# Kernel tuning notes

Measured on AMD Instinct MI355X. Metric: run time of the kernel, lower is better.

## Reference

```python
import jax, jax.numpy as jnp
import numpy as np

N = 100000      # nodes
E = 1600000     # directed edges (before self-loops)
F_IN, H1, H2 = 128, 64, 32


def setup_inputs() -> dict:
    key = jax.random.key(0)
    ks = jax.random.split(key, 8)
    x = jax.random.normal(ks[0], (N, F_IN), dtype=jnp.float32)
    edge_index = jax.random.randint(ks[1], (2, E), 0, N, dtype=jnp.int32)
    # GCNConv lin weights (no bias in lin; separate additive bias), glorot-ish scale
    W1 = jax.random.normal(ks[2], (F_IN, H1), dtype=jnp.float32) / np.sqrt(F_IN)
    b1 = jnp.zeros((H1,), dtype=jnp.float32)
    W2 = jax.random.normal(ks[3], (H1, H2), dtype=jnp.float32) / np.sqrt(H1)
    b2 = jnp.zeros((H2,), dtype=jnp.float32)
    Wfc = jax.random.normal(ks[4], (H2, 1), dtype=jnp.float32) / np.sqrt(H2)
    bfc = jnp.zeros((1,), dtype=jnp.float32)
    return {"x": x, "edge_index": edge_index, "W1": W1, "b1": b1,
            "W2": W2, "b2": b2, "Wfc": Wfc, "bfc": bfc}


def _gcn_norm(edge_index):
    # PyG GCNConv default: add self-loops, symmetric normalization D^-1/2 (A+I) D^-1/2
    loop = jnp.arange(N, dtype=edge_index.dtype)
    src = jnp.concatenate([edge_index[0], loop])
    dst = jnp.concatenate([edge_index[1], loop])
    deg = jax.ops.segment_sum(jnp.ones_like(dst, dtype=jnp.float32), dst, num_segments=N)
    dinv = jnp.where(deg > 0, jax.lax.rsqrt(deg), 0.0)
    norm = dinv[src] * dinv[dst]  # [E+N]
    return src, dst, norm


def _gcn_conv(x, W, b, src, dst, norm):
    h = x @ W                                 # project first (PyG order)
    msg = norm[:, None] * h[src]              # gather + scale
    agg = jax.ops.segment_sum(msg, dst, num_segments=N)  # scatter-add
    return agg + b


def reference(x, edge_index, W1, b1, W2, b2, Wfc, bfc):
    src, dst, norm = _gcn_norm(edge_index)
    h = jax.nn.relu(_gcn_conv(x, W1, b1, src, dst, norm))
    h = jax.nn.relu(_gcn_conv(h, W2, b2, src, dst, norm))
    return h @ Wfc + bfc
```

## Files before the change

### kernel.cpp

```cpp
#include <hip/hip_runtime.h>

#define N_NODES 100000
#define BSH 9
#define NBKT ((N_NODES + 511) >> BSH)
#define CH 7168

typedef unsigned int u32;
typedef unsigned short u16;
typedef __attribute__((ext_vector_type(8))) short s8v;
typedef __attribute__((ext_vector_type(4))) float f4v;

static __device__ __forceinline__ u16 f2bf(float f) {
    union { float f; u32 u; } c; c.f = f;
    u32 r = (c.u + 0x7fffu + ((c.u >> 16) & 1u)) >> 16;
    return (u16)r;
}
static __device__ __forceinline__ float bf2f_u(u16 h) {
    union { u32 u; float f; } c; c.u = ((u32)h) << 16;
    return c.f;
}
static __device__ __forceinline__ void acc2(u32 p, float& a, float& b) {
    union { u32 u; float f; } lo, hi;
    lo.u = p << 16;
    hi.u = p & 0xffff0000u;
    a += lo.f;
    b += hi.f;
}


__global__ __launch_bounds__(256) void coarsehist_k(const int* __restrict__ dst,
        int* __restrict__ ccount, int E, int TOT) {
    __shared__ int hist[256];
    hist[threadIdx.x] = 0;
    __syncthreads();
    int base = blockIdx.x * CH;
    int cnt = min(CH, TOT - base);
    for (int i = threadIdx.x; i < cnt; i += 256) {
        int e = base + i;
        int d = (e < E) ? dst[e] : e - E;
        atomicAdd(&hist[d >> BSH], 1);
    }
    __syncthreads();
    if (hist[threadIdx.x]) atomicAdd(&ccount[threadIdx.x], hist[threadIdx.x]);
}

__global__ __launch_bounds__(256) void coarsescan_k(const int* __restrict__ ccount,
        int* __restrict__ cbase, int* __restrict__ bcur, int* __restrict__ offsets) {
    __shared__ int ps[256];
    int t = threadIdx.x;
    int c = (t < NBKT) ? ccount[t] : 0;
    ps[t] = c;
    __syncthreads();
    for (int off = 1; off < 256; off <<= 1) {
        int val = ps[t];
        int add = (t >= off) ? ps[t - off] : 0;
        __syncthreads();
        ps[t] = val + add;
        __syncthreads();
    }
    int incl = ps[t], excl = incl - c;
    if (t < NBKT) cbase[t] = excl;
    bcur[t] = (t < NBKT) ? excl : incl;
    if (t == NBKT - 1) cbase[NBKT] = incl;
    if (t == 255) offsets[N_NODES] = ps[255];
}

__global__ __launch_bounds__(256) void partition_k(const int* __restrict__ src,
        const int* __restrict__ dst, int* __restrict__ bcur,
        uint2* __restrict__ bktBuf, int E, int TOT) {
    __shared__ int hist[256];
    __shared__ int lbase[256];
    __shared__ int gbase[256];
    __shared__ int ps[256];
    __shared__ uint2 stage[CH];
    int t = threadIdx.x;
    int base = blockIdx.x * CH;
    int cnt = min(CH, TOT - base);
    hist[t] = 0;
    __syncthreads();
    for (int i = t; i < cnt; i += 256) {
        int e = base + i;
        int d = (e < E) ? dst[e] : e - E;
        atomicAdd(&hist[d >> BSH], 1);
    }
    __syncthreads();
    ps[t] = hist[t];
    __syncthreads();
    for (int off = 1; off < 256; off <<= 1) {
        int val = ps[t];
        int add = (t >= off) ? ps[t - off] : 0;
        __syncthreads();
        ps[t] = val + add;
        __syncthreads();
    }
    lbase[t] = ps[t] - hist[t];
    gbase[t] = atomicAdd(&bcur[t], hist[t]);
    hist[t] = 0;
    __syncthreads();
    for (int i = t; i < cnt; i += 256) {
        int e = base + i;
        int s, d;
        if (e < E) { s = src[e]; d = dst[e]; }
        else       { s = d = e - E; }
        int b = d >> BSH;
        int lpos = lbase[b] + atomicAdd(&hist[b], 1);
        stage[lpos] = make_uint2((u32)s, (u32)d);
    }
    __syncthreads();
    for (int i = t; i < cnt; i += 256) {
        uint2 p = stage[i];
        int b = (int)p.y >> BSH;
        bktBuf[gbase[b] + (i - lbase[b])] = p;
    }
}

__global__ __launch_bounds__(256) void buildfill_k(const int* __restrict__ cbase,
        const uint2* __restrict__ bktBuf, int* __restrict__ offsets,
        float* __restrict__ dinv, int* __restrict__ srt_src) {
    __shared__ int hist[512];
    __shared__ int hscan[512];
    __shared__ int cur[512];
    __shared__ int ps[256];
    int t = threadIdx.x;
    int b = blockIdx.x;
    int v0 = b << BSH;
    int nv = min(512, N_NODES - v0);
    hist[t] = 0; hist[t + 256] = 0;
    cur[t] = 0;  cur[t + 256] = 0;
    __syncthreads();
    int beg = cbase[b], endi = cbase[b + 1];
    for (int i = beg + t; i < endi; i += 256)
        atomicAdd(&hist[(int)bktBuf[i].y - v0], 1);
    __syncthreads();
    int a = hist[2 * t], bb = hist[2 * t + 1];
    int own = a + bb;
    ps[t] = own;
    __syncthreads();
    for (int off = 1; off < 256; off <<= 1) {
        int val = ps[t];
        int add = (t >= off) ? ps[t - off] : 0;
        __syncthreads();
        ps[t] = val + add;
        __syncthreads();
    }
    int excl2 = ps[t] - own;
    hscan[2 * t] = excl2;
    hscan[2 * t + 1] = excl2 + a;
    __syncthreads();
    for (int j = t; j < nv; j += 256) {
        offsets[v0 + j] = beg + hscan[j];
        dinv[v0 + j] = rsqrtf((float)hist[j]);
    }
    for (int i = beg + t; i < endi; i += 256) {
        uint2 p = bktBuf[i];
        int j = (int)p.y - v0;
        int pos = atomicAdd(&cur[j], 1);
        srt_src[beg + hscan[j] + pos] = (int)p.x;
    }
}


static __device__ __forceinline__ void split8(const float* __restrict__ xp,
                                              s8v& hi, s8v& lo) {
    float4 v0 = *(const float4*)xp;
    float4 v1 = *(const float4*)(xp + 4);
    float xv[8] = {v0.x, v0.y, v0.z, v0.w, v1.x, v1.y, v1.z, v1.w};
#pragma unroll
    for (int j = 0; j < 8; ++j) {
        u16 h = f2bf(xv[j]);
        hi[j] = (short)h;
        lo[j] = (short)f2bf(xv[j] - bf2f_u(h));
    }
}

__global__ __launch_bounds__(256) void gemm1_k(const float* __restrict__ x,
                                               const float* __restrict__ W1,
                                               const float* __restrict__ dinv,
                                               u16* __restrict__ h1b) {
    __shared__ __attribute__((aligned(16))) short Bs[2][4][4][512];
    int t = threadIdx.x;
    for (int i = t; i < 128 * 64; i += 256) {
        int k = i >> 6, c = i & 63;
        float w = W1[i];
        u16 h = f2bf(w);
        u16 l = f2bf(w - bf2f_u(h));
        int ks = k >> 5, kg = (k >> 3) & 3, kk = k & 7;
        int ct = c >> 4, col = c & 15;
        int idx = (kg * 16 + col) * 8 + kk;
        Bs[0][ks][ct][idx] = (short)h;
        Bs[1][ks][ct][idx] = (short)l;
    }
    __syncthreads();

    int lane = t & 63;
    int rows0 = (blockIdx.x * 4 + (t >> 6)) * 32;
    if (rows0 >= N_NODES) return;

    f4v acc[2][4];
#pragma unroll
    for (int rt = 0; rt < 2; ++rt)
#pragma unroll
        for (int ct = 0; ct < 4; ++ct)
            acc[rt][ct] = (f4v){0.f, 0.f, 0.f, 0.f};

    int arow = lane & 15;
    int kgl = lane >> 4;
#pragma unroll
    for (int ks = 0; ks < 4; ++ks) {
        s8v bh[4], bl[4];
#pragma unroll
        for (int ct = 0; ct < 4; ++ct) {
            bh[ct] = *(const s8v*)&Bs[0][ks][ct][lane * 8];
            bl[ct] = *(const s8v*)&Bs[1][ks][ct][lane * 8];
        }
#pragma unroll
        for (int rt = 0; rt < 2; ++rt) {
            s8v ah, al;
            const float* xp = x + (size_t)(rows0 + rt * 16 + arow) * 128
                                + ks * 32 + kgl * 8;
            split8(xp, ah, al);
#pragma unroll
            for (int ct = 0; ct < 4; ++ct) {
                acc[rt][ct] = __builtin_amdgcn_mfma_f32_16x16x32_bf16(
                    ah, bh[ct], acc[rt][ct], 0, 0, 0);
                acc[rt][ct] = __builtin_amdgcn_mfma_f32_16x16x32_bf16(
                    ah, bl[ct], acc[rt][ct], 0, 0, 0);
                acc[rt][ct] = __builtin_amdgcn_mfma_f32_16x16x32_bf16(
                    al, bh[ct], acc[rt][ct], 0, 0, 0);
            }
        }
    }

#pragma unroll
    for (int rt = 0; rt < 2; ++rt) {
        int rbase = rows0 + rt * 16 + ((lane >> 4) << 2);
        float dv[4];
#pragma unroll
        for (int r = 0; r < 4; ++r) dv[r] = dinv[rbase + r];
#pragma unroll
        for (int ct = 0; ct < 4; ++ct) {
            int col = ct * 16 + (lane & 15);
#pragma unroll
            for (int r = 0; r < 4; ++r)
                h1b[(size_t)(rbase + r) * 64 + col] = f2bf(acc[rt][ct][r] * dv[r]);
        }
    }
}


__global__ __launch_bounds__(256) void layer2_k(const int* __restrict__ offsets,
        const int* __restrict__ srt_src, const float* __restrict__ dinv,
        const u16* __restrict__ h1b, const float* __restrict__ b1,
        const float* __restrict__ W2, u16* __restrict__ h2b) {
    __shared__ float W2s[64 * 32];
    __shared__ float b1s[64];
    for (int i = threadIdx.x; i < 64 * 32; i += 256) W2s[i] = W2[i];
    if (threadIdx.x < 64) b1s[threadIdx.x] = b1[threadIdx.x];
    __syncthreads();
    int lane = threadIdx.x & 63;
    int f = lane & 15, q = lane >> 4;
    int v0 = blockIdx.x * 8 + (threadIdx.x >> 6) * 2;
    int v1 = v0 + 1;
    int i0 = offsets[v0], e0 = offsets[v1], e1 = offsets[v1 + 1];
    int i1 = e0;
    const uint2* rows = (const uint2*)h1b;
    float a0 = 0.f, a1 = 0.f, a2 = 0.f, a3 = 0.f;
    float c0 = 0.f, c1 = 0.f, c2 = 0.f, c3 = 0.f;
    while (i0 + 8 <= e0 && i1 + 8 <= e1) {
        int sA = srt_src[i0 + q];
        int sB = srt_src[i0 + 4 + q];
        int sC = srt_src[i1 + q];
        int sD = srt_src[i1 + 4 + q];
        uint2 pA = rows[sA * 16 + f];
        uint2 pB = rows[sB * 16 + f];
        uint2 pC = rows[sC * 16 + f];
        uint2 pD = rows[sD * 16 + f];
        acc2(pA.x, a0, a1); acc2(pA.y, a2, a3);
        acc2(pB.x, a0, a1); acc2(pB.y, a2, a3);
        acc2(pC.x, c0, c1); acc2(pC.y, c2, c3);
        acc2(pD.x, c0, c1); acc2(pD.y, c2, c3);
        i0 += 8; i1 += 8;
    }
    for (; i0 + 8 <= e0; i0 += 8) {
        int sA = srt_src[i0 + q], sB = srt_src[i0 + 4 + q];
        uint2 pA = rows[sA * 16 + f], pB = rows[sB * 16 + f];
        acc2(pA.x, a0, a1); acc2(pA.y, a2, a3);
        acc2(pB.x, a0, a1); acc2(pB.y, a2, a3);
    }
    for (; i0 < e0; i0 += 4) {
        int j = i0 + q;
        if (j < e0) {
            int s = srt_src[j];
            uint2 p = rows[s * 16 + f];
            acc2(p.x, a0, a1); acc2(p.y, a2, a3);
        }
    }
    for (; i1 + 8 <= e1; i1 += 8) {
        int sA = srt_src[i1 + q], sB = srt_src[i1 + 4 + q];
        uint2 pA = rows[sA * 16 + f], pB = rows[sB * 16 + f];
        acc2(pA.x, c0, c1); acc2(pA.y, c2, c3);
        acc2(pB.x, c0, c1); acc2(pB.y, c2, c3);
    }
    for (; i1 < e1; i1 += 4) {
        int j = i1 + q;
        if (j < e1) {
            int s = srt_src[j];
            uint2 p = rows[s * 16 + f];
            acc2(p.x, c0, c1); acc2(p.y, c2, c3);
        }
    }
    a0 += __shfl_xor(a0, 16, 64); a0 += __shfl_xor(a0, 32, 64);
    a1 += __shfl_xor(a1, 16, 64); a1 += __shfl_xor(a1, 32, 64);
    a2 += __shfl_xor(a2, 16, 64); a2 += __shfl_xor(a2, 32, 64);
    a3 += __shfl_xor(a3, 16, 64); a3 += __shfl_xor(a3, 32, 64);
    c0 += __shfl_xor(c0, 16, 64); c0 += __shfl_xor(c0, 32, 64);
    c1 += __shfl_xor(c1, 16, 64); c1 += __shfl_xor(c1, 32, 64);
    c2 += __shfl_xor(c2, 16, 64); c2 += __shfl_xor(c2, 32, 64);
    c3 += __shfl_xor(c3, 16, 64); c3 += __shfl_xor(c3, 32, 64);
    bool lo = (lane < 32);
    float dv = lo ? dinv[v0] : dinv[v1];
    float t0 = lo ? a0 : c0;
    float t1 = lo ? a1 : c1;
    float t2 = lo ? a2 : c2;
    float t3 = lo ? a3 : c3;
    float r0 = fmaxf(fmaf(dv, t0, b1s[4 * f + 0]), 0.f);
    float r1 = fmaxf(fmaf(dv, t1, b1s[4 * f + 1]), 0.f);
    float r2 = fmaxf(fmaf(dv, t2, b1s[4 * f + 2]), 0.f);
    float r3 = fmaxf(fmaf(dv, t3, b1s[4 * f + 3]), 0.f);
    int c = lane & 31;
    float o = 0.f;
#pragma unroll
    for (int j2 = 0; j2 < 16; ++j2) {
        float R0 = __shfl(r0, j2, 16);
        float R1 = __shfl(r1, j2, 16);
        float R2 = __shfl(r2, j2, 16);
        float R3 = __shfl(r3, j2, 16);
        o = fmaf(R0, W2s[(4 * j2 + 0) * 32 + c], o);
        o = fmaf(R1, W2s[(4 * j2 + 1) * 32 + c], o);
        o = fmaf(R2, W2s[(4 * j2 + 2) * 32 + c], o);
        o = fmaf(R3, W2s[(4 * j2 + 3) * 32 + c], o);
    }
    int vst = lo ? v0 : v1;
    h2b[vst * 32 + c] = f2bf(dv * o);
}


#define GATH3(ii, A, B, C, D) { \
    int s_ = srt_src[(ii) + oc]; \
    uint2 p_ = rows[s_ * 8 + f]; \
    acc2(p_.x, A, B); acc2(p_.y, C, D); }

__global__ __launch_bounds__(256) void layer3_k(const int* __restrict__ offsets,
        const int* __restrict__ srt_src, const float* __restrict__ dinv,
        const u16* __restrict__ h2b, const float* __restrict__ b2,
        const float* __restrict__ Wfc, const float* __restrict__ bfc,
        float* __restrict__ out) {
    int lane = threadIdx.x & 63;
    int f = lane & 7, oc = lane >> 3;
    int vb = blockIdx.x * 16 + (threadIdx.x >> 6) * 4;
    int o0 = offsets[vb], o1 = offsets[vb + 1], o2 = offsets[vb + 2];
    int o3 = offsets[vb + 3], o4 = offsets[vb + 4];
    int i0 = o0, e0 = o1, i1 = o1, e1 = o2, i2 = o2, e2 = o3, i3 = o3, e3 = o4;
    const uint2* rows = (const uint2*)h2b;
    float A0=0.f,A1=0.f,A2=0.f,A3=0.f, B0=0.f,B1=0.f,B2=0.f,B3=0.f;
    float C0=0.f,C1=0.f,C2=0.f,C3=0.f, D0=0.f,D1=0.f,D2=0.f,D3=0.f;
    while (i0 + 8 <= e0 && i1 + 8 <= e1 && i2 + 8 <= e2 && i3 + 8 <= e3) {
        GATH3(i0, A0, A1, A2, A3);
        GATH3(i1, B0, B1, B2, B3);
        GATH3(i2, C0, C1, C2, C3);
        GATH3(i3, D0, D1, D2, D3);
        i0 += 8; i1 += 8; i2 += 8; i3 += 8;
    }
    while (i0 + 8 <= e0) { GATH3(i0, A0, A1, A2, A3); i0 += 8; }
    if (i0 + oc < e0)    { GATH3(i0, A0, A1, A2, A3); }
    while (i1 + 8 <= e1) { GATH3(i1, B0, B1, B2, B3); i1 += 8; }
    if (i1 + oc < e1)    { GATH3(i1, B0, B1, B2, B3); }
    while (i2 + 8 <= e2) { GATH3(i2, C0, C1, C2, C3); i2 += 8; }
    if (i2 + oc < e2)    { GATH3(i2, C0, C1, C2, C3); }
    while (i3 + 8 <= e3) { GATH3(i3, D0, D1, D2, D3); i3 += 8; }
    if (i3 + oc < e3)    { GATH3(i3, D0, D1, D2, D3); }
#define RED3(X) X += __shfl_xor(X, 8, 64); X += __shfl_xor(X, 16, 64); X += __shfl_xor(X, 32, 64)
    RED3(A0); RED3(A1); RED3(A2); RED3(A3);
    RED3(B0); RED3(B1); RED3(B2); RED3(B3);
    RED3(C0); RED3(C1); RED3(C2); RED3(C3);
    RED3(D0); RED3(D1); RED3(D2); RED3(D3);
    float w0 = Wfc[4 * f + 0], w1 = Wfc[4 * f + 1];
    float w2 = Wfc[4 * f + 2], w3 = Wfc[4 * f + 3];
    float g0 = b2[4 * f + 0], g1 = b2[4 * f + 1];
    float g2 = b2[4 * f + 2], g3 = b2[4 * f + 3];
    float dv0 = dinv[vb], dv1 = dinv[vb + 1], dv2 = dinv[vb + 2], dv3 = dinv[vb + 3];
    float p0 = fmaxf(fmaf(dv0, A0, g0), 0.f) * w0 + fmaxf(fmaf(dv0, A1, g1), 0.f) * w1
             + fmaxf(fmaf(dv0, A2, g2), 0.f) * w2 + fmaxf(fmaf(dv0, A3, g3), 0.f) * w3;
    float p1 = fmaxf(fmaf(dv1, B0, g0), 0.f) * w0 + fmaxf(fmaf(dv1, B1, g1), 0.f) * w1
             + fmaxf(fmaf(dv1, B2, g2), 0.f) * w2 + fmaxf(fmaf(dv1, B3, g3), 0.f) * w3;
    float p2 = fmaxf(fmaf(dv2, C0, g0), 0.f) * w0 + fmaxf(fmaf(dv2, C1, g1), 0.f) * w1
             + fmaxf(fmaf(dv2, C2, g2), 0.f) * w2 + fmaxf(fmaf(dv2, C3, g3), 0.f) * w3;
    float p3 = fmaxf(fmaf(dv3, D0, g0), 0.f) * w0 + fmaxf(fmaf(dv3, D1, g1), 0.f) * w1
             + fmaxf(fmaf(dv3, D2, g2), 0.f) * w2 + fmaxf(fmaf(dv3, D3, g3), 0.f) * w3;
#define REDP(X) X += __shfl_xor(X, 1, 64); X += __shfl_xor(X, 2, 64); X += __shfl_xor(X, 4, 64)
    REDP(p0); REDP(p1); REDP(p2); REDP(p3);
    if (lane == 0) {
        float bb = bfc[0];
        out[vb + 0] = p0 + bb;
        out[vb + 1] = p1 + bb;
        out[vb + 2] = p2 + bb;
        out[vb + 3] = p3 + bb;
    }
}


extern "C" void kernel_launch(void* const* d_in, const int* in_sizes, int n_in,
                              void* d_out, int out_size, void* d_ws, size_t ws_size,
                              hipStream_t stream) {
    const float* x   = (const float*)d_in[0];
    const int*   ei  = (const int*)d_in[1];
    const float* W1  = (const float*)d_in[2];
    const float* b1  = (const float*)d_in[3];
    const float* W2  = (const float*)d_in[4];
    const float* b2  = (const float*)d_in[5];
    const float* Wfc = (const float*)d_in[6];
    const float* bfc = (const float*)d_in[7];
    float* out = (float*)d_out;

    const int E = in_sizes[1] / 2;
    const int TOT = E + N_NODES;
    const int* src = ei;
    const int* dst = ei + E;

    int*   ccount  = (int*)d_ws;
    int*   cbase   = ccount + 256;
    int*   bcur    = cbase + 256;
    int*   offsets = bcur + 256;
    int*   srt_src = offsets + N_NODES + 1;
    size_t bb_off  = (size_t)(srt_src - (int*)d_ws) + TOT;
    bb_off = (bb_off + 1) & ~(size_t)1;
    uint2* bktBuf  = (uint2*)((int*)d_ws + bb_off);
    float* dinv    = (float*)((int*)d_ws + bb_off + 2 * (size_t)TOT);
    u16*   h1b     = (u16*)(dinv + N_NODES);
    u16*   h2b     = h1b + (size_t)N_NODES * 64;

    const int NCH = (TOT + CH - 1) / CH;

    hipMemsetAsync(ccount, 0, 256 * sizeof(int), stream);
    coarsehist_k<<<NCH, 256, 0, stream>>>(dst, ccount, E, TOT);
    coarsescan_k<<<1, 256, 0, stream>>>(ccount, cbase, bcur, offsets);
    partition_k<<<NCH, 256, 0, stream>>>(src, dst, bcur, bktBuf, E, TOT);
    buildfill_k<<<NBKT, 256, 0, stream>>>(cbase, bktBuf, offsets, dinv, srt_src);

    const int GB1 = (N_NODES / 32 + 3) / 4;
    gemm1_k<<<GB1, 256, 0, stream>>>(x, W1, dinv, h1b);

    layer2_k<<<N_NODES / 8, 256, 0, stream>>>(offsets, srt_src, dinv, h1b, b1, W2, h2b);
    layer3_k<<<N_NODES / 16, 256, 0, stream>>>(offsets, srt_src, dinv, h2b, b2, Wfc,
                                               bfc, out);
}
```

Before: 210.2 us.

## Widen gathers to 16-byte loads and software-pipeline edge fetches in aggregation kernels

Layer2 and layer3 gather kernels now load bf16 feature rows as uint4 (8 bf16 per lane) instead of uint2, so each wave covers more edges per iteration (8 in layer2, 16 in layer3). A register double-buffer prefetches the next gather before accumulating the current one, keeping more loads in flight. The intent is to cut instruction count and hide gather latency. It costs more registers and larger shuffle reductions, which may lower occupancy and waste lanes on low-degree nodes.

```diff
diff --git a/kernel.cpp b/kernel.cpp
--- a/kernel.cpp
+++ b/kernel.cpp
@@ -25,6 +25,10 @@
     hi.u = p & 0xffff0000u;
     a += lo.f;
     b += hi.f;
+}
+static __device__ __forceinline__ void acc8(uint4 p, float* a) {
+    acc2(p.x, a[0], a[1]); acc2(p.y, a[2], a[3]);
+    acc2(p.z, a[4], a[5]); acc2(p.w, a[6], a[7]);
 }
 
 
@@ -248,6 +252,10 @@
 }
 
 
+#define L2_FETCH(F, V, P, EE) \
+    if (P + 8 <= EE) { int s_ = srt_src[P + oc8]; F = rows4[s_ * 8 + f8]; \
+                       V = true; P += 8; } else V = false;
+
 __global__ __launch_bounds__(256) void layer2_k(const int* __restrict__ offsets,
         const int* __restrict__ srt_src, const float* __restrict__ dinv,
         const u16* __restrict__ h1b, const float* __restrict__ b1,
@@ -258,97 +266,71 @@
     if (threadIdx.x < 64) b1s[threadIdx.x] = b1[threadIdx.x];
     __syncthreads();
     int lane = threadIdx.x & 63;
-    int f = lane & 15, q = lane >> 4;
+    int f8 = lane & 7, oc8 = lane >> 3;
     int v0 = blockIdx.x * 8 + (threadIdx.x >> 6) * 2;
     int v1 = v0 + 1;
-    int i0 = offsets[v0], e0 = offsets[v1], e1 = offsets[v1 + 1];
-    int i1 = e0;
-    const uint2* rows = (const uint2*)h1b;
-    float a0 = 0.f, a1 = 0.f, a2 = 0.f, a3 = 0.f;
-    float c0 = 0.f, c1 = 0.f, c2 = 0.f, c3 = 0.f;
-    while (i0 + 8 <= e0 && i1 + 8 <= e1) {
-        int sA = srt_src[i0 + q];
-        int sB = srt_src[i0 + 4 + q];
-        int sC = srt_src[i1 + q];
-        int sD = srt_src[i1 + 4 + q];
-        uint2 pA = rows[sA * 16 + f];
-        uint2 pB = rows[sB * 16 + f];
-        uint2 pC = rows[sC * 16 + f];
-        uint2 pD = rows[sD * 16 + f];
-        acc2(pA.x, a0, a1); acc2(pA.y, a2, a3);
-        acc2(pB.x, a0, a1); acc2(pB.y, a2, a3);
-        acc2(pC.x, c0, c1); acc2(pC.y, c2, c3);
-        acc2(pD.x, c0, c1); acc2(pD.y, c2, c3);
-        i0 += 8; i1 += 8;
-    }
-    for (; i0 + 8 <= e0; i0 += 8) {
-        int sA = srt_src[i0 + q], sB = srt_src[i0 + 4 + q];
-        uint2 pA = rows[sA * 16 + f], pB = rows[sB * 16 + f];
-        acc2(pA.x, a0, a1); acc2(pA.y, a2, a3);
-        acc2(pB.x, a0, a1); acc2(pB.y, a2, a3);
-    }
-    for (; i0 < e0; i0 += 4) {
-        int j = i0 + q;
-        if (j < e0) {
-            int s = srt_src[j];
-            uint2 p = rows[s * 16 + f];
-            acc2(p.x, a0, a1); acc2(p.y, a2, a3);
-        }
-    }
-    for (; i1 + 8 <= e1; i1 += 8) {
-        int sA = srt_src[i1 + q], sB = srt_src[i1 + 4 + q];
-        uint2 pA = rows[sA * 16 + f], pB = rows[sB * 16 + f];
-        acc2(pA.x, c0, c1); acc2(pA.y, c2, c3);
-        acc2(pB.x, c0, c1); acc2(pB.y, c2, c3);
-    }
-    for (; i1 < e1; i1 += 4) {
-        int j = i1 + q;
-        if (j < e1) {
-            int s = srt_src[j];
-            uint2 p = rows[s * 16 + f];
-            acc2(p.x, c0, c1); acc2(p.y, c2, c3);
-        }
-    }
-    a0 += __shfl_xor(a0, 16, 64); a0 += __shfl_xor(a0, 32, 64);
-    a1 += __shfl_xor(a1, 16, 64); a1 += __shfl_xor(a1, 32, 64);
-    a2 += __shfl_xor(a2, 16, 64); a2 += __shfl_xor(a2, 32, 64);
-    a3 += __shfl_xor(a3, 16, 64); a3 += __shfl_xor(a3, 32, 64);
-    c0 += __shfl_xor(c0, 16, 64); c0 += __shfl_xor(c0, 32, 64);
-    c1 += __shfl_xor(c1, 16, 64); c1 += __shfl_xor(c1, 32, 64);
-    c2 += __shfl_xor(c2, 16, 64); c2 += __shfl_xor(c2, 32, 64);
-    c3 += __shfl_xor(c3, 16, 64); c3 += __shfl_xor(c3, 32, 64);
+    int p0 = offsets[v0], e0 = offsets[v1], e1 = offsets[v1 + 1];
+    int p1 = e0;
+    const uint4* rows4 = (const uint4*)h1b;
+    float a[8] = {0.f, 0.f, 0.f, 0.f, 0.f, 0.f, 0.f, 0.f};
+    float c[8] = {0.f, 0.f, 0.f, 0.f, 0.f, 0.f, 0.f, 0.f};
+    uint4 F0a, F0b, F1a, F1b;
+    bool v0a, v0b, v1a, v1b;
+    L2_FETCH(F0a, v0a, p0, e0);
+    L2_FETCH(F1a, v1a, p1, e1);
+    L2_FETCH(F0b, v0b, p0, e0);
+    L2_FETCH(F1b, v1b, p1, e1);
+    while (v0a || v1a) {
+        uint4 C0 = F0a, C1 = F1a;
+        bool c0 = v0a, c1 = v1a;
+        F0a = F0b; v0a = v0b;
+        F1a = F1b; v1a = v1b;
+        L2_FETCH(F0b, v0b, p0, e0);
+        L2_FETCH(F1b, v1b, p1, e1);
+        if (c0) acc8(C0, a);
+        if (c1) acc8(C1, c);
+    }
+    if (p0 + oc8 < e0) {
+        int s_ = srt_src[p0 + oc8];
+        acc8(rows4[s_ * 8 + f8], a);
+    }
+    if (p1 + oc8 < e1) {
+        int s_ = srt_src[p1 + oc8];
+        acc8(rows4[s_ * 8 + f8], c);
+    }
+#pragma unroll
+    for (int j = 0; j < 8; ++j) {
+        a[j] += __shfl_xor(a[j], 8, 64);
+        a[j] += __shfl_xor(a[j], 16, 64);
+        a[j] += __shfl_xor(a[j], 32, 64);
+        c[j] += __shfl_xor(c[j], 8, 64);
+        c[j] += __shfl_xor(c[j], 16, 64);
+        c[j] += __shfl_xor(c[j], 32, 64);
+    }
     bool lo = (lane < 32);
     float dv = lo ? dinv[v0] : dinv[v1];
-    float t0 = lo ? a0 : c0;
-    float t1 = lo ? a1 : c1;
-    float t2 = lo ? a2 : c2;
-    float t3 = lo ? a3 : c3;
-    float r0 = fmaxf(fmaf(dv, t0, b1s[4 * f + 0]), 0.f);
-    float r1 = fmaxf(fmaf(dv, t1, b1s[4 * f + 1]), 0.f);
-    float r2 = fmaxf(fmaf(dv, t2, b1s[4 * f + 2]), 0.f);
-    float r3 = fmaxf(fmaf(dv, t3, b1s[4 * f + 3]), 0.f);
-    int c = lane & 31;
+    float r[8];
+#pragma unroll
+    for (int j = 0; j < 8; ++j) {
+        float tv = lo ? a[j] : c[j];
+        r[j] = fmaxf(fmaf(dv, tv, b1s[8 * f8 + j]), 0.f);
+    }
+    int cc = lane & 31;
     float o = 0.f;
 #pragma unroll
-    for (int j2 = 0; j2 < 16; ++j2) {
-        float R0 = __shfl(r0, j2, 16);
-        float R1 = __shfl(r1, j2, 16);
-        float R2 = __shfl(r2, j2, 16);
-        float R3 = __shfl(r3, j2, 16);
-        o = fmaf(R0, W2s[(4 * j2 + 0) * 32 + c], o);
-        o = fmaf(R1, W2s[(4 * j2 + 1) * 32 + c], o);
-        o = fmaf(R2, W2s[(4 * j2 + 2) * 32 + c], o);
-        o = fmaf(R3, W2s[(4 * j2 + 3) * 32 + c], o);
+    for (int g = 0; g < 8; ++g) {
+#pragma unroll
+        for (int j = 0; j < 8; ++j)
+            o = fmaf(__shfl(r[j], g, 8), W2s[(8 * g + j) * 32 + cc], o);
     }
     int vst = lo ? v0 : v1;
-    h2b[vst * 32 + c] = f2bf(dv * o);
-}
-
-
-#define GATH3(ii, A, B, C, D) { \
-    int s_ = srt_src[(ii) + oc]; \
-    uint2 p_ = rows[s_ * 8 + f]; \
-    acc2(p_.x, A, B); acc2(p_.y, C, D); }
+    h2b[vst * 32 + cc] = f2bf(dv * o);
+}
+
+
+#define L3_FETCH(F, V, P, EE) \
+    if (P + 16 <= EE) { int s_ = srt_src[P + sl]; F = rows4[s_ * 4 + f4]; \
+                        V = true; P += 16; } else V = false;
 
 __global__ __launch_bounds__(256) void layer3_k(const int* __restrict__ offsets,
         const int* __restrict__ srt_src, const float* __restrict__ dinv,
@@ -356,55 +338,70 @@
         const float* __restrict__ Wfc, const float* __restrict__ bfc,
         float* __restrict__ out) {
     int lane = threadIdx.x & 63;
-    int f = lane & 7, oc = lane >> 3;
+    int f4 = lane & 3, sl = lane >> 2;
     int vb = blockIdx.x * 16 + (threadIdx.x >> 6) * 4;
     int o0 = offsets[vb], o1 = offsets[vb + 1], o2 = offsets[vb + 2];
     int o3 = offsets[vb + 3], o4 = offsets[vb + 4];
-    int i0 = o0, e0 = o1, i1 = o1, e1 = o2, i2 = o2, e2 = o3, i3 = o3, e3 = o4;
-    const uint2* rows = (const uint2*)h2b;
-    float A0=0.f,A1=0.f,A2=0.f,A3=0.f, B0=0.f,B1=0.f,B2=0.f,B3=0.f;
-    float C0=0.f,C1=0.f,C2=0.f,C3=0.f, D0=0.f,D1=0.f,D2=0.f,D3=0.f;
-    while (i0 + 8 <= e0 && i1 + 8 <= e1 && i2 + 8 <= e2 && i3 + 8 <= e3) {
-        GATH3(i0, A0, A1, A2, A3);
-        GATH3(i1, B0, B1, B2, B3);
-        GATH3(i2, C0, C1, C2, C3);
-        GATH3(i3, D0, D1, D2, D3);
-        i0 += 8; i1 += 8; i2 += 8; i3 += 8;
-    }
-    while (i0 + 8 <= e0) { GATH3(i0, A0, A1, A2, A3); i0 += 8; }
-    if (i0 + oc < e0)    { GATH3(i0, A0, A1, A2, A3); }
-    while (i1 + 8 <= e1) { GATH3(i1, B0, B1, B2, B3); i1 += 8; }
-    if (i1 + oc < e1)    { GATH3(i1, B0, B1, B2, B3); }
-    while (i2 + 8 <= e2) { GATH3(i2, C0, C1, C2, C3); i2 += 8; }
-    if (i2 + oc < e2)    { GATH3(i2, C0, C1, C2, C3); }
-    while (i3 + 8 <= e3) { GATH3(i3, D0, D1, D2, D3); i3 += 8; }
-    if (i3 + oc < e3)    { GATH3(i3, D0, D1, D2, D3); }
-#define RED3(X) X += __shfl_xor(X, 8, 64); X += __shfl_xor(X, 16, 64); X += __shfl_xor(X, 32, 64)
-    RED3(A0); RED3(A1); RED3(A2); RED3(A3);
-    RED3(B0); RED3(B1); RED3(B2); RED3(B3);
-    RED3(C0); RED3(C1); RED3(C2); RED3(C3);
-    RED3(D0); RED3(D1); RED3(D2); RED3(D3);
-    float w0 = Wfc[4 * f + 0], w1 = Wfc[4 * f + 1];
-    float w2 = Wfc[4 * f + 2], w3 = Wfc[4 * f + 3];
-    float g0 = b2[4 * f + 0], g1 = b2[4 * f + 1];
-    float g2 = b2[4 * f + 2], g3 = b2[4 * f + 3];
+    int p0 = o0, e0 = o1, p1 = o1, e1 = o2, p2 = o2, e2 = o3, p3 = o3, e3 = o4;
+    const uint4* rows4 = (const uint4*)h2b;
+    float A[8] = {0.f, 0.f, 0.f, 0.f, 0.f, 0.f, 0.f, 0.f};
+    float B[8] = {0.f, 0.f, 0.f, 0.f, 0.f, 0.f, 0.f, 0.f};
+    float C[8] = {0.f, 0.f, 0.f, 0.f, 0.f, 0.f, 0.f, 0.f};
+    float D[8] = {0.f, 0.f, 0.f, 0.f, 0.f, 0.f, 0.f, 0.f};
+    uint4 F0, F1, F2, F3;
+    bool g0, g1, g2, g3;
+    L3_FETCH(F0, g0, p0, e0);
+    L3_FETCH(F1, g1, p1, e1);
+    L3_FETCH(F2, g2, p2, e2);
+    L3_FETCH(F3, g3, p3, e3);
+    while (g0 || g1 || g2 || g3) {
+        uint4 T0 = F0, T1 = F1, T2 = F2, T3 = F3;
+        bool h0 = g0, h1 = g1, h2 = g2, h3 = g3;
+        L3_FETCH(F0, g0, p0, e0);
+        L3_FETCH(F1, g1, p1, e1);
+        L3_FETCH(F2, g2, p2, e2);
+        L3_FETCH(F3, g3, p3, e3);
+        if (h0) acc8(T0, A);
+        if (h1) acc8(T1, B);
+        if (h2) acc8(T2, C);
+        if (h3) acc8(T3, D);
+    }
+    if (p0 + sl < e0) { int s_ = srt_src[p0 + sl]; acc8(rows4[s_ * 4 + f4], A); }
+    if (p1 + sl < e1) { int s_ = srt_src[p1 + sl]; acc8(rows4[s_ * 4 + f4], B); }
+    if (p2 + sl < e2) { int s_ = srt_src[p2 + sl]; acc8(rows4[s_ * 4 + f4], C); }
+    if (p3 + sl < e3) { int s_ = srt_src[p3 + sl]; acc8(rows4[s_ * 4 + f4], D); }
+#pragma unroll
+    for (int j = 0; j < 8; ++j) {
+        A[j] += __shfl_xor(A[j], 4, 64);  A[j] += __shfl_xor(A[j], 8, 64);
+        A[j] += __shfl_xor(A[j], 16, 64); A[j] += __shfl_xor(A[j], 32, 64);
+        B[j] += __shfl_xor(B[j], 4, 64);  B[j] += __shfl_xor(B[j], 8, 64);
+        B[j] += __shfl_xor(B[j], 16, 64); B[j] += __shfl_xor(B[j], 32, 64);
+        C[j] += __shfl_xor(C[j], 4, 64);  C[j] += __shfl_xor(C[j], 8, 64);
+        C[j] += __shfl_xor(C[j], 16, 64); C[j] += __shfl_xor(C[j], 32, 64);
+        D[j] += __shfl_xor(D[j], 4, 64);  D[j] += __shfl_xor(D[j], 8, 64);
+        D[j] += __shfl_xor(D[j], 16, 64); D[j] += __shfl_xor(D[j], 32, 64);
+    }
     float dv0 = dinv[vb], dv1 = dinv[vb + 1], dv2 = dinv[vb + 2], dv3 = dinv[vb + 3];
-    float p0 = fmaxf(fmaf(dv0, A0, g0), 0.f) * w0 + fmaxf(fmaf(dv0, A1, g1), 0.f) * w1
-             + fmaxf(fmaf(dv0, A2, g2), 0.f) * w2 + fmaxf(fmaf(dv0, A3, g3), 0.f) * w3;
-    float p1 = fmaxf(fmaf(dv1, B0, g0), 0.f) * w0 + fmaxf(fmaf(dv1, B1, g1), 0.f) * w1
-             + fmaxf(fmaf(dv1, B2, g2), 0.f) * w2 + fmaxf(fmaf(dv1, B3, g3), 0.f) * w3;
-    float p2 = fmaxf(fmaf(dv2, C0, g0), 0.f) * w0 + fmaxf(fmaf(dv2, C1, g1), 0.f) * w1
-             + fmaxf(fmaf(dv2, C2, g2), 0.f) * w2 + fmaxf(fmaf(dv2, C3, g3), 0.f) * w3;
-    float p3 = fmaxf(fmaf(dv3, D0, g0), 0.f) * w0 + fmaxf(fmaf(dv3, D1, g1), 0.f) * w1
-             + fmaxf(fmaf(dv3, D2, g2), 0.f) * w2 + fmaxf(fmaf(dv3, D3, g3), 0.f) * w3;
-#define REDP(X) X += __shfl_xor(X, 1, 64); X += __shfl_xor(X, 2, 64); X += __shfl_xor(X, 4, 64)
-    REDP(p0); REDP(p1); REDP(p2); REDP(p3);
+    float pr0 = 0.f, pr1 = 0.f, pr2 = 0.f, pr3 = 0.f;
+#pragma unroll
+    for (int j = 0; j < 8; ++j) {
+        int k = 8 * f4 + j;
+        float w = Wfc[k], g = b2[k];
+        pr0 += fmaxf(fmaf(dv0, A[j], g), 0.f) * w;
+        pr1 += fmaxf(fmaf(dv1, B[j], g), 0.f) * w;
+        pr2 += fmaxf(fmaf(dv2, C[j], g), 0.f) * w;
+        pr3 += fmaxf(fmaf(dv3, D[j], g), 0.f) * w;
+    }
+    pr0 += __shfl_xor(pr0, 1, 64); pr0 += __shfl_xor(pr0, 2, 64);
+    pr1 += __shfl_xor(pr1, 1, 64); pr1 += __shfl_xor(pr1, 2, 64);
+    pr2 += __shfl_xor(pr2, 1, 64); pr2 += __shfl_xor(pr2, 2, 64);
+    pr3 += __shfl_xor(pr3, 1, 64); pr3 += __shfl_xor(pr3, 2, 64);
     if (lane == 0) {
         float bb = bfc[0];
-        out[vb + 0] = p0 + bb;
-        out[vb + 1] = p1 + bb;
-        out[vb + 2] = p2 + bb;
-        out[vb + 3] = p3 + bb;
+        out[vb + 0] = pr0 + bb;
+        out[vb + 1] = pr1 + bb;
+        out[vb + 2] = pr2 + bb;
+        out[vb + 3] = pr3 + bb;
     }
 }
 
```

Measured after the change: 226.3 us. 1.08x slower.

## Split layer-2 aggregation into source-range segments for cache locality

Applied to the files above, without the earlier changes.

Sorts each node's incoming edges by source segment (src>>15, four segments) during CSR build. The layer-2 gather then runs one pass per segment, with blocks interleaved so concurrently running blocks read from the same quarter of h1b and hit in L2 more often. Each pass writes bf16 partial sums, and a new finalize kernel adds the four partials, applies bias, ReLU and the W2 projection. The cost is an extra partial buffer of roughly 51MB, an extra kernel launch, larger shared histograms in buildfill, and an extra bf16 rounding of the partial sums.

```diff
diff --git a/kernel.cpp b/kernel.cpp
--- a/kernel.cpp
+++ b/kernel.cpp
@@ -4,6 +4,8 @@
 #define BSH 9
 #define NBKT ((N_NODES + 511) >> BSH)
 #define CH 7168
+#define SEGSH 15
+#define NSEG 4
 
 typedef unsigned int u32;
 typedef unsigned short u16;
@@ -25,6 +27,10 @@
     hi.u = p & 0xffff0000u;
     a += lo.f;
     b += hi.f;
+}
+static __device__ __forceinline__ void acc8(uint4 p, float* a) {
+    acc2(p.x, a[0], a[1]); acc2(p.y, a[2], a[3]);
+    acc2(p.z, a[4], a[5]); acc2(p.w, a[6], a[7]);
 }
 
 
@@ -116,24 +122,28 @@
 
 __global__ __launch_bounds__(256) void buildfill_k(const int* __restrict__ cbase,
         const uint2* __restrict__ bktBuf, int* __restrict__ offsets,
-        float* __restrict__ dinv, int* __restrict__ srt_src) {
-    __shared__ int hist[512];
-    __shared__ int hscan[512];
-    __shared__ int cur[512];
+        int* __restrict__ soff, float* __restrict__ dinv,
+        int* __restrict__ srt_src) {
+    __shared__ int hist[2048];
+    __shared__ int hscan[2048];
+    __shared__ int cur[2048];
     __shared__ int ps[256];
     int t = threadIdx.x;
     int b = blockIdx.x;
     int v0 = b << BSH;
     int nv = min(512, N_NODES - v0);
-    hist[t] = 0; hist[t + 256] = 0;
-    cur[t] = 0;  cur[t + 256] = 0;
+    for (int k = t; k < 2048; k += 256) { hist[k] = 0; cur[k] = 0; }
     __syncthreads();
     int beg = cbase[b], endi = cbase[b + 1];
-    for (int i = beg + t; i < endi; i += 256)
-        atomicAdd(&hist[(int)bktBuf[i].y - v0], 1);
-    __syncthreads();
-    int a = hist[2 * t], bb = hist[2 * t + 1];
-    int own = a + bb;
+    for (int i = beg + t; i < endi; i += 256) {
+        uint2 p = bktBuf[i];
+        atomicAdd(&hist[(((int)p.y - v0) << 2) | ((int)p.x >> SEGSH)], 1);
+    }
+    __syncthreads();
+    int loc[8];
+    int own = 0;
+#pragma unroll
+    for (int k = 0; k < 8; ++k) { loc[k] = hist[8 * t + k]; own += loc[k]; }
     ps[t] = own;
     __syncthreads();
     for (int off = 1; off < 256; off <<= 1) {
@@ -143,19 +153,24 @@
         ps[t] = val + add;
         __syncthreads();
     }
-    int excl2 = ps[t] - own;
-    hscan[2 * t] = excl2;
-    hscan[2 * t + 1] = excl2 + a;
+    int run = ps[t] - own;
+#pragma unroll
+    for (int k = 0; k < 8; ++k) { hscan[8 * t + k] = run; run += loc[k]; }
     __syncthreads();
     for (int j = t; j < nv; j += 256) {
-        offsets[v0 + j] = beg + hscan[j];
-        dinv[v0 + j] = rsqrtf((float)hist[j]);
+        int h4 = j << 2;
+        offsets[v0 + j] = beg + hscan[h4];
+#pragma unroll
+        for (int s = 0; s < 4; ++s)
+            soff[(size_t)(v0 + j) * 4 + s] = beg + hscan[h4 + s];
+        dinv[v0 + j] = rsqrtf((float)(hist[h4] + hist[h4 + 1]
+                                      + hist[h4 + 2] + hist[h4 + 3]));
     }
     for (int i = beg + t; i < endi; i += 256) {
         uint2 p = bktBuf[i];
-        int j = (int)p.y - v0;
-        int pos = atomicAdd(&cur[j], 1);
-        srt_src[beg + hscan[j] + pos] = (int)p.x;
+        int j2 = (((int)p.y - v0) << 2) | ((int)p.x >> SEGSH);
+        int pos = atomicAdd(&cur[j2], 1);
+        srt_src[beg + hscan[j2] + pos] = (int)p.x;
     }
 }
 
@@ -248,66 +263,52 @@
 }
 
 
-__global__ __launch_bounds__(256) void layer2_k(const int* __restrict__ offsets,
-        const int* __restrict__ srt_src, const float* __restrict__ dinv,
-        const u16* __restrict__ h1b, const float* __restrict__ b1,
-        const float* __restrict__ W2, u16* __restrict__ h2b) {
-    __shared__ float W2s[64 * 32];
-    __shared__ float b1s[64];
-    for (int i = threadIdx.x; i < 64 * 32; i += 256) W2s[i] = W2[i];
-    if (threadIdx.x < 64) b1s[threadIdx.x] = b1[threadIdx.x];
-    __syncthreads();
-    int lane = threadIdx.x & 63;
+__global__ __launch_bounds__(256) void aggseg_k(const int* __restrict__ soff,
+        const int* __restrict__ offsets, const int* __restrict__ srt_src,
+        const u16* __restrict__ h1b, u16* __restrict__ partial) {
+    int t = threadIdx.x, lane = t & 63;
+    int b = blockIdx.x;
+    int r = b & 7;
+    int seg = r >> 1;
+    int ng = (b >> 3) * 2 + (r & 1);
+    int v0 = ng * 8 + (t >> 6) * 2;
+    int v1 = v0 + 1;
     int f = lane & 15, q = lane >> 4;
-    int v0 = blockIdx.x * 8 + (threadIdx.x >> 6) * 2;
-    int v1 = v0 + 1;
-    int i0 = offsets[v0], e0 = offsets[v1], e1 = offsets[v1 + 1];
-    int i1 = e0;
+    int i0 = soff[(size_t)v0 * 4 + seg];
+    int e0 = (seg < 3) ? soff[(size_t)v0 * 4 + seg + 1] : offsets[v0 + 1];
+    int i1 = soff[(size_t)v1 * 4 + seg];
+    int e1 = (seg < 3) ? soff[(size_t)v1 * 4 + seg + 1] : offsets[v1 + 1];
     const uint2* rows = (const uint2*)h1b;
     float a0 = 0.f, a1 = 0.f, a2 = 0.f, a3 = 0.f;
     float c0 = 0.f, c1 = 0.f, c2 = 0.f, c3 = 0.f;
-    while (i0 + 8 <= e0 && i1 + 8 <= e1) {
+    while (i0 + 4 <= e0 && i1 + 4 <= e1) {
         int sA = srt_src[i0 + q];
-        int sB = srt_src[i0 + 4 + q];
         int sC = srt_src[i1 + q];
-        int sD = srt_src[i1 + 4 + q];
         uint2 pA = rows[sA * 16 + f];
-        uint2 pB = rows[sB * 16 + f];
         uint2 pC = rows[sC * 16 + f];
-        uint2 pD = rows[sD * 16 + f];
         acc2(pA.x, a0, a1); acc2(pA.y, a2, a3);
-        acc2(pB.x, a0, a1); acc2(pB.y, a2, a3);
         acc2(pC.x, c0, c1); acc2(pC.y, c2, c3);
-        acc2(pD.x, c0, c1); acc2(pD.y, c2, c3);
-        i0 += 8; i1 += 8;
-    }
-    for (; i0 + 8 <= e0; i0 += 8) {
-        int sA = srt_src[i0 + q], sB = srt_src[i0 + 4 + q];
-        uint2 pA = rows[sA * 16 + f], pB = rows[sB * 16 + f];
-        acc2(pA.x, a0, a1); acc2(pA.y, a2, a3);
-        acc2(pB.x, a0, a1); acc2(pB.y, a2, a3);
-    }
-    for (; i0 < e0; i0 += 4) {
-        int j = i0 + q;
-        if (j < e0) {
-            int s = srt_src[j];
-            uint2 p = rows[s * 16 + f];
-            acc2(p.x, a0, a1); acc2(p.y, a2, a3);
-        }
-    }
-    for (; i1 + 8 <= e1; i1 += 8) {
-        int sA = srt_src[i1 + q], sB = srt_src[i1 + 4 + q];
-        uint2 pA = rows[sA * 16 + f], pB = rows[sB * 16 + f];
-        acc2(pA.x, c0, c1); acc2(pA.y, c2, c3);
-        acc2(pB.x, c0, c1); acc2(pB.y, c2, c3);
-    }
-    for (; i1 < e1; i1 += 4) {
-        int j = i1 + q;
-        if (j < e1) {
-            int s = srt_src[j];
-            uint2 p = rows[s * 16 + f];
-            acc2(p.x, c0, c1); acc2(p.y, c2, c3);
-        }
+        i0 += 4; i1 += 4;
+    }
+    for (; i0 + 4 <= e0; i0 += 4) {
+        int s = srt_src[i0 + q];
+        uint2 p = rows[s * 16 + f];
+        acc2(p.x, a0, a1); acc2(p.y, a2, a3);
+    }
+    if (i0 + q < e0) {
+        int s = srt_src[i0 + q];
+        uint2 p = rows[s * 16 + f];
+        acc2(p.x, a0, a1); acc2(p.y, a2, a3);
+    }
+    for (; i1 + 4 <= e1; i1 += 4) {
+        int s = srt_src[i1 + q];
+        uint2 p = rows[s * 16 + f];
+        acc2(p.x, c0, c1); acc2(p.y, c2, c3);
+    }
+    if (i1 + q < e1) {
+        int s = srt_src[i1 + q];
+        uint2 p = rows[s * 16 + f];
+        acc2(p.x, c0, c1); acc2(p.y, c2, c3);
     }
     a0 += __shfl_xor(a0, 16, 64); a0 += __shfl_xor(a0, 32, 64);
     a1 += __shfl_xor(a1, 16, 64); a1 += __shfl_xor(a1, 32, 64);
@@ -318,30 +319,51 @@
     c2 += __shfl_xor(c2, 16, 64); c2 += __shfl_xor(c2, 32, 64);
     c3 += __shfl_xor(c3, 16, 64); c3 += __shfl_xor(c3, 32, 64);
     bool lo = (lane < 32);
-    float dv = lo ? dinv[v0] : dinv[v1];
+    int v = lo ? v0 : v1;
     float t0 = lo ? a0 : c0;
     float t1 = lo ? a1 : c1;
     float t2 = lo ? a2 : c2;
     float t3 = lo ? a3 : c3;
-    float r0 = fmaxf(fmaf(dv, t0, b1s[4 * f + 0]), 0.f);
-    float r1 = fmaxf(fmaf(dv, t1, b1s[4 * f + 1]), 0.f);
-    float r2 = fmaxf(fmaf(dv, t2, b1s[4 * f + 2]), 0.f);
-    float r3 = fmaxf(fmaf(dv, t3, b1s[4 * f + 3]), 0.f);
-    int c = lane & 31;
+    if ((lane & 31) < 16) {
+        u32 xw = (u32)f2bf(t0) | ((u32)f2bf(t1) << 16);
+        u32 yw = (u32)f2bf(t2) | ((u32)f2bf(t3) << 16);
+        ((uint2*)partial)[((size_t)seg * N_NODES + v) * 16 + (lane & 15)] =
+            make_uint2(xw, yw);
+    }
+}
+
+
+__global__ __launch_bounds__(256) void l2fin_k(const u16* __restrict__ partial,
+        const float* __restrict__ dinv, const float* __restrict__ b1,
+        const float* __restrict__ W2, u16* __restrict__ h2b) {
+    __shared__ float W2s[64 * 32];
+    __shared__ float b1s[64];
+    for (int i = threadIdx.x; i < 64 * 32; i += 256) W2s[i] = W2[i];
+    if (threadIdx.x < 64) b1s[threadIdx.x] = b1[threadIdx.x];
+    __syncthreads();
+    int t = threadIdx.x, lane = t & 63;
+    int half = lane >> 5, fl = lane & 31;
+    int v = blockIdx.x * 8 + (t >> 6) * 2 + half;
+    const u32* prow = (const u32*)partial;
+    float r0 = 0.f, r1 = 0.f;
+#pragma unroll
+    for (int s = 0; s < 4; ++s) {
+        u32 u = prow[((size_t)s * N_NODES + v) * 32 + fl];
+        r0 += bf2f_u((u16)(u & 0xffff));
+        r1 += bf2f_u((u16)(u >> 16));
+    }
+    float dv = dinv[v];
+    r0 = fmaxf(fmaf(dv, r0, b1s[2 * fl]), 0.f);
+    r1 = fmaxf(fmaf(dv, r1, b1s[2 * fl + 1]), 0.f);
     float o = 0.f;
 #pragma unroll
-    for (int j2 = 0; j2 < 16; ++j2) {
-        float R0 = __shfl(r0, j2, 16);
-        float R1 = __shfl(r1, j2, 16);
-        float R2 = __shfl(r2, j2, 16);
-        float R3 = __shfl(r3, j2, 16);
-        o = fmaf(R0, W2s[(4 * j2 + 0) * 32 + c], o);
-        o = fmaf(R1, W2s[(4 * j2 + 1) * 32 + c], o);
-        o = fmaf(R2, W2s[(4 * j2 + 2) * 32 + c], o);
-        o = fmaf(R3, W2s[(4 * j2 + 3) * 32 + c], o);
-    }
-    int vst = lo ? v0 : v1;
-    h2b[vst * 32 + c] = f2bf(dv * o);
+    for (int g = 0; g < 32; ++g) {
+        float R0 = __shfl(r0, g, 32);
+        float R1 = __shfl(r1, g, 32);
+        o = fmaf(R0, W2s[(2 * g) * 32 + fl], o);
+        o = fmaf(R1, W2s[(2 * g + 1) * 32 + fl], o);
+    }
+    h2b[(size_t)v * 32 + fl] = f2bf(dv * o);
 }
 
 
@@ -431,13 +453,14 @@
     int*   cbase   = ccount + 256;
     int*   bcur    = cbase + 256;
     int*   offsets = bcur + 256;
-    int*   srt_src = offsets + N_NODES + 1;
-    size_t bb_off  = (size_t)(srt_src - (int*)d_ws) + TOT;
-    bb_off = (bb_off + 1) & ~(size_t)1;
-    uint2* bktBuf  = (uint2*)((int*)d_ws + bb_off);
-    float* dinv    = (float*)((int*)d_ws + bb_off + 2 * (size_t)TOT);
+    int*   soff    = offsets + N_NODES + 1;
+    int*   srt_src = soff + 4 * N_NODES;
+    float* dinv    = (float*)(srt_src + TOT);
     u16*   h1b     = (u16*)(dinv + N_NODES);
     u16*   h2b     = h1b + (size_t)N_NODES * 64;
+    size_t tail = ((size_t)(h2b + (size_t)N_NODES * 32 - (u16*)d_ws) + 3) & ~(size_t)3;
+    u16*   partial = (u16*)d_ws + tail;
+    uint2* bktBuf  = (uint2*)partial;
 
     const int NCH = (TOT + CH - 1) / CH;
 
@@ -445,12 +468,14 @@
     coarsehist_k<<<NCH, 256, 0, stream>>>(dst, ccount, E, TOT);
     coarsescan_k<<<1, 256, 0, stream>>>(ccount, cbase, bcur, offsets);
     partition_k<<<NCH, 256, 0, stream>>>(src, dst, bcur, bktBuf, E, TOT);
-    buildfill_k<<<NBKT, 256, 0, stream>>>(cbase, bktBuf, offsets, dinv, srt_src);
+    buildfill_k<<<NBKT, 256, 0, stream>>>(cbase, bktBuf, offsets, soff, dinv, srt_src);
 
     const int GB1 = (N_NODES / 32 + 3) / 4;
     gemm1_k<<<GB1, 256, 0, stream>>>(x, W1, dinv, h1b);
 
-    layer2_k<<<N_NODES / 8, 256, 0, stream>>>(offsets, srt_src, dinv, h1b, b1, W2, h2b);
+    aggseg_k<<<NSEG * (N_NODES / 8), 256, 0, stream>>>(soff, offsets, srt_src,
+                                                       h1b, partial);
+    l2fin_k<<<N_NODES / 8, 256, 0, stream>>>(partial, dinv, b1, W2, h2b);
     layer3_k<<<N_NODES / 16, 256, 0, stream>>>(offsets, srt_src, dinv, h2b, b2, Wfc,
                                                bfc, out);
 }
```

Measured after the change: 252.9 us. +20.3%, slower.

## Replace coarse histogram pass with fixed-slack buckets and pack edge pairs

Applied to the files above, without the earlier changes.

Drops the coarse histogram kernel, the scan kernel and the memset. Each destination bucket now gets a fixed SLACK-sized region, so partitioning needs one pass over the edges instead of two. Bucket entries are packed into one 32-bit word (9-bit local dst plus 17-bit src) instead of a uint2, which halves bucket-buffer traffic. Because the CSR now has gaps between buckets, per-node end indices are stored and used by the aggregation kernels. This relies on no bucket overflowing 10240 entries, which holds for uniformly random inputs but is not guaranteed in general.

```diff
diff --git a/kernel.cpp b/kernel.cpp
--- a/kernel.cpp
+++ b/kernel.cpp
@@ -4,9 +4,11 @@
 #define BSH 9
 #define NBKT ((N_NODES + 511) >> BSH)
 #define CH 7168
+#define SLACK 10240
 
 typedef unsigned int u32;
 typedef unsigned short u16;
+typedef unsigned char u8;
 typedef __attribute__((ext_vector_type(8))) short s8v;
 typedef __attribute__((ext_vector_type(4))) float f4v;
 
@@ -26,53 +28,25 @@
     a += lo.f;
     b += hi.f;
 }
-
-
-__global__ __launch_bounds__(256) void coarsehist_k(const int* __restrict__ dst,
-        int* __restrict__ ccount, int E, int TOT) {
-    __shared__ int hist[256];
-    hist[threadIdx.x] = 0;
-    __syncthreads();
-    int base = blockIdx.x * CH;
-    int cnt = min(CH, TOT - base);
-    for (int i = threadIdx.x; i < cnt; i += 256) {
-        int e = base + i;
-        int d = (e < E) ? dst[e] : e - E;
-        atomicAdd(&hist[d >> BSH], 1);
-    }
-    __syncthreads();
-    if (hist[threadIdx.x]) atomicAdd(&ccount[threadIdx.x], hist[threadIdx.x]);
-}
-
-__global__ __launch_bounds__(256) void coarsescan_k(const int* __restrict__ ccount,
-        int* __restrict__ cbase, int* __restrict__ bcur, int* __restrict__ offsets) {
-    __shared__ int ps[256];
-    int t = threadIdx.x;
-    int c = (t < NBKT) ? ccount[t] : 0;
-    ps[t] = c;
-    __syncthreads();
-    for (int off = 1; off < 256; off <<= 1) {
-        int val = ps[t];
-        int add = (t >= off) ? ps[t - off] : 0;
-        __syncthreads();
-        ps[t] = val + add;
-        __syncthreads();
-    }
-    int incl = ps[t], excl = incl - c;
-    if (t < NBKT) cbase[t] = excl;
-    bcur[t] = (t < NBKT) ? excl : incl;
-    if (t == NBKT - 1) cbase[NBKT] = incl;
-    if (t == 255) offsets[N_NODES] = ps[255];
+static __device__ __forceinline__ void acc8(uint4 p, float* a) {
+    acc2(p.x, a[0], a[1]); acc2(p.y, a[2], a[3]);
+    acc2(p.z, a[4], a[5]); acc2(p.w, a[6], a[7]);
+}
+
+
+__global__ __launch_bounds__(256) void initcur_k(int* __restrict__ bcur) {
+    bcur[threadIdx.x] = threadIdx.x * SLACK;
 }
 
 __global__ __launch_bounds__(256) void partition_k(const int* __restrict__ src,
         const int* __restrict__ dst, int* __restrict__ bcur,
-        uint2* __restrict__ bktBuf, int E, int TOT) {
+        u32* __restrict__ bktBuf, int E, int TOT) {
     __shared__ int hist[256];
     __shared__ int lbase[256];
     __shared__ int gbase[256];
     __shared__ int ps[256];
-    __shared__ uint2 stage[CH];
+    __shared__ u32 stage[CH];
+    __shared__ u8 stageB[CH];
     int t = threadIdx.x;
     int base = blockIdx.x * CH;
     int cnt = min(CH, TOT - base);
@@ -104,19 +78,20 @@
         else       { s = d = e - E; }
         int b = d >> BSH;
         int lpos = lbase[b] + atomicAdd(&hist[b], 1);
-        stage[lpos] = make_uint2((u32)s, (u32)d);
+        stage[lpos] = ((u32)(d & 511) << 17) | (u32)s;
+        stageB[lpos] = (u8)b;
     }
     __syncthreads();
     for (int i = t; i < cnt; i += 256) {
-        uint2 p = stage[i];
-        int b = (int)p.y >> BSH;
-        bktBuf[gbase[b] + (i - lbase[b])] = p;
-    }
-}
-
-__global__ __launch_bounds__(256) void buildfill_k(const int* __restrict__ cbase,
-        const uint2* __restrict__ bktBuf, int* __restrict__ offsets,
-        float* __restrict__ dinv, int* __restrict__ srt_src) {
+        int b = stageB[i];
+        bktBuf[gbase[b] + (i - lbase[b])] = stage[i];
+    }
+}
+
+__global__ __launch_bounds__(256) void buildfill_k(const int* __restrict__ bcur,
+        const u32* __restrict__ bktBuf, int* __restrict__ offsets,
+        int* __restrict__ ends, float* __restrict__ dinv,
+        int* __restrict__ srt_src) {
     __shared__ int hist[512];
     __shared__ int hscan[512];
     __shared__ int cur[512];
@@ -125,12 +100,13 @@
     int b = blockIdx.x;
     int v0 = b << BSH;
     int nv = min(512, N_NODES - v0);
+    int base = b * SLACK;
+    int cnt = bcur[b] - base;
     hist[t] = 0; hist[t + 256] = 0;
     cur[t] = 0;  cur[t + 256] = 0;
     __syncthreads();
-    int beg = cbase[b], endi = cbase[b + 1];
-    for (int i = beg + t; i < endi; i += 256)
-        atomicAdd(&hist[(int)bktBuf[i].y - v0], 1);
+    for (int i = t; i < cnt; i += 256)
+        atomicAdd(&hist[bktBuf[base + i] >> 17], 1);
     __syncthreads();
     int a = hist[2 * t], bb = hist[2 * t + 1];
     int own = a + bb;
@@ -148,14 +124,16 @@
     hscan[2 * t + 1] = excl2 + a;
     __syncthreads();
     for (int j = t; j < nv; j += 256) {
-        offsets[v0 + j] = beg + hscan[j];
+        int o = base + hscan[j];
+        offsets[v0 + j] = o;
+        ends[v0 + j] = o + hist[j];
         dinv[v0 + j] = rsqrtf((float)hist[j]);
     }
-    for (int i = beg + t; i < endi; i += 256) {
-        uint2 p = bktBuf[i];
-        int j = (int)p.y - v0;
+    for (int i = t; i < cnt; i += 256) {
+        u32 it = bktBuf[base + i];
+        int j = it >> 17;
         int pos = atomicAdd(&cur[j], 1);
-        srt_src[beg + hscan[j] + pos] = (int)p.x;
+        srt_src[base + hscan[j] + pos] = (int)(it & 0x1ffffu);
     }
 }
 
@@ -249,9 +227,10 @@
 
 
 __global__ __launch_bounds__(256) void layer2_k(const int* __restrict__ offsets,
-        const int* __restrict__ srt_src, const float* __restrict__ dinv,
-        const u16* __restrict__ h1b, const float* __restrict__ b1,
-        const float* __restrict__ W2, u16* __restrict__ h2b) {
+        const int* __restrict__ ends, const int* __restrict__ srt_src,
+        const float* __restrict__ dinv, const u16* __restrict__ h1b,
+        const float* __restrict__ b1, const float* __restrict__ W2,
+        u16* __restrict__ h2b) {
     __shared__ float W2s[64 * 32];
     __shared__ float b1s[64];
     for (int i = threadIdx.x; i < 64 * 32; i += 256) W2s[i] = W2[i];
@@ -261,8 +240,8 @@
     int f = lane & 15, q = lane >> 4;
     int v0 = blockIdx.x * 8 + (threadIdx.x >> 6) * 2;
     int v1 = v0 + 1;
-    int i0 = offsets[v0], e0 = offsets[v1], e1 = offsets[v1 + 1];
-    int i1 = e0;
+    int i0 = offsets[v0], e0 = ends[v0];
+    int i1 = offsets[v1], e1 = ends[v1];
     const uint2* rows = (const uint2*)h1b;
     float a0 = 0.f, a1 = 0.f, a2 = 0.f, a3 = 0.f;
     float c0 = 0.f, c1 = 0.f, c2 = 0.f, c3 = 0.f;
@@ -351,16 +330,17 @@
     acc2(p_.x, A, B); acc2(p_.y, C, D); }
 
 __global__ __launch_bounds__(256) void layer3_k(const int* __restrict__ offsets,
-        const int* __restrict__ srt_src, const float* __restrict__ dinv,
-        const u16* __restrict__ h2b, const float* __restrict__ b2,
-        const float* __restrict__ Wfc, const float* __restrict__ bfc,
-        float* __restrict__ out) {
+        const int* __restrict__ ends, const int* __restrict__ srt_src,
+        const float* __restrict__ dinv, const u16* __restrict__ h2b,
+        const float* __restrict__ b2, const float* __restrict__ Wfc,
+        const float* __restrict__ bfc, float* __restrict__ out) {
     int lane = threadIdx.x & 63;
     int f = lane & 7, oc = lane >> 3;
     int vb = blockIdx.x * 16 + (threadIdx.x >> 6) * 4;
-    int o0 = offsets[vb], o1 = offsets[vb + 1], o2 = offsets[vb + 2];
-    int o3 = offsets[vb + 3], o4 = offsets[vb + 4];
-    int i0 = o0, e0 = o1, i1 = o1, e1 = o2, i2 = o2, e2 = o3, i3 = o3, e3 = o4;
+    int i0 = offsets[vb],     e0 = ends[vb];
+    int i1 = offsets[vb + 1], e1 = ends[vb + 1];
+    int i2 = offsets[vb + 2], e2 = ends[vb + 2];
+    int i3 = offsets[vb + 3], e3 = ends[vb + 3];
     const uint2* rows = (const uint2*)h2b;
     float A0=0.f,A1=0.f,A2=0.f,A3=0.f, B0=0.f,B1=0.f,B2=0.f,B3=0.f;
     float C0=0.f,C1=0.f,C2=0.f,C3=0.f, D0=0.f,D1=0.f,D2=0.f,D3=0.f;
@@ -427,30 +407,27 @@
     const int* src = ei;
     const int* dst = ei + E;
 
-    int*   ccount  = (int*)d_ws;
-    int*   cbase   = ccount + 256;
-    int*   bcur    = cbase + 256;
+    int*   bcur    = (int*)d_ws;
     int*   offsets = bcur + 256;
-    int*   srt_src = offsets + N_NODES + 1;
-    size_t bb_off  = (size_t)(srt_src - (int*)d_ws) + TOT;
-    bb_off = (bb_off + 1) & ~(size_t)1;
-    uint2* bktBuf  = (uint2*)((int*)d_ws + bb_off);
-    float* dinv    = (float*)((int*)d_ws + bb_off + 2 * (size_t)TOT);
+    int*   ends    = offsets + N_NODES;
+    int*   srt_src = ends + N_NODES;
+    u32*   bktBuf  = (u32*)(srt_src + NBKT * SLACK);
+    float* dinv    = (float*)(bktBuf + NBKT * SLACK);
     u16*   h1b     = (u16*)(dinv + N_NODES);
     u16*   h2b     = h1b + (size_t)N_NODES * 64;
 
     const int NCH = (TOT + CH - 1) / CH;
 
-    hipMemsetAsync(ccount, 0, 256 * sizeof(int), stream);
-    coarsehist_k<<<NCH, 256, 0, stream>>>(dst, ccount, E, TOT);
-    coarsescan_k<<<1, 256, 0, stream>>>(ccount, cbase, bcur, offsets);
+    initcur_k<<<1, 256, 0, stream>>>(bcur);
     partition_k<<<NCH, 256, 0, stream>>>(src, dst, bcur, bktBuf, E, TOT);
-    buildfill_k<<<NBKT, 256, 0, stream>>>(cbase, bktBuf, offsets, dinv, srt_src);
+    buildfill_k<<<NBKT, 256, 0, stream>>>(bcur, bktBuf, offsets, ends, dinv,
+                                          srt_src);
 
     const int GB1 = (N_NODES / 32 + 3) / 4;
     gemm1_k<<<GB1, 256, 0, stream>>>(x, W1, dinv, h1b);
 
-    layer2_k<<<N_NODES / 8, 256, 0, stream>>>(offsets, srt_src, dinv, h1b, b1, W2, h2b);
-    layer3_k<<<N_NODES / 16, 256, 0, stream>>>(offsets, srt_src, dinv, h2b, b2, Wfc,
-                                               bfc, out);
-}
+    layer2_k<<<N_NODES / 8, 256, 0, stream>>>(offsets, ends, srt_src, dinv, h1b,
+                                              b1, W2, h2b);
+    layer3_k<<<N_NODES / 16, 256, 0, stream>>>(offsets, ends, srt_src, dinv, h2b,
+                                               b2, Wfc, bfc, out);
+}
```

After: 187.7 us. 1.12x faster.
